# Kernel optimization log

Hardware: AMD Instinct MI355X
Metric: run time of the kernel (lower is better)

The kernel has to match this reference:

```python
import jax, jax.numpy as jnp
import numpy as np

N_NODES = 100000
N_EDGES = 1600000
HIDDEN = 128


def setup_inputs() -> dict:
    key = jax.random.key(0)
    k_x, k_w1, k_w2, k_v, k_i, k_o = jax.random.split(key, 6)
    x = jax.random.normal(k_x, (N_NODES, HIDDEN), dtype=jnp.float32)
    # gate1/gate2 are Linear(hidden,1,bias=False); store their weight rows as vectors
    w1 = jax.random.normal(k_w1, (HIDDEN,), dtype=jnp.float32) * 0.1
    w2 = jax.random.normal(k_w2, (HIDDEN,), dtype=jnp.float32) * 0.1
    adj_vals = jax.random.uniform(k_v, (N_EDGES,), dtype=jnp.float32)
    in_idx = jax.random.randint(k_i, (N_EDGES,), 0, N_NODES, dtype=jnp.int32)
    out_idx = jax.random.randint(k_o, (N_EDGES,), 0, N_NODES, dtype=jnp.int32)
    return {"x": x, "w1": w1, "w2": w2, "adj_vals": adj_vals,
            "in_idx": in_idx, "out_idx": out_idx}


def reference(x, w1, w2, adj_vals, in_idx, out_idx):
    # per-node gate scalars: x1 = gate1(x), x2 = gate2(x)  -> [N]
    x1 = x @ w1
    x2 = x @ w2
    # edge gate: tanh(x1[src] + x2[dst]) * adj_value  (dropout is identity in eval mode)
    m = jnp.tanh(x1[in_idx] + x2[out_idx]) * adj_vals  # [E]
    # sparse.mm(adj_alpha, x): out[i] = sum_{e: row(e)=i} m_e * x[col(e)]
    messages = m[:, None] * x[out_idx]                 # [E, d]
    result = jax.ops.segment_sum(messages, in_idx, num_segments=N_NODES)
    return result
```

## Files before the change

### kernel.cpp

```cpp
#include <hip/hip_runtime.h>

#define N_NODES 100000
#define N_EDGES 1600000
#define HIDDEN  128

#define NPB_SHIFT 9
#define NPB       512
#define NB        ((N_NODES + NPB - 1) / NPB)
#define PART_T    512
#define PART_EPT  16
#define PART_EPB  (PART_T * PART_EPT)
#define PART_B    ((N_EDGES + PART_EPB - 1) / PART_EPB)
#define HIST_EPT  16
#define HIST_EPB  (256 * HIST_EPT)
#define HIST_B    ((N_EDGES + HIST_EPB - 1) / HIST_EPB)
#define GATES_B   ((N_NODES * 32 + 255) / 256)
#define FINE_PE   20

#define SCAN_C 16
#define SCAN_T ((N_NODES + SCAN_C - 1) / SCAN_C)
#define SCAN_THREADS 6400
#define SCAN_B (SCAN_THREADS / 256)

__device__ __forceinline__ ushort f2bf(float f) {
    unsigned int u = __float_as_uint(f);
    u = (u + 0x7FFFu + ((u >> 16) & 1u)) >> 16;
    return (ushort)u;
}

__global__ void fagcn_zero(int* __restrict__ bcnt) {
    const int t = (int)threadIdx.x;
    if (t < NB) bcnt[t] = 0;
}

__global__ void fagcn_gates_hist(const float* __restrict__ x,
                                 const float* __restrict__ w1,
                                 const float* __restrict__ w2,
                                 const int*   __restrict__ in_idx,
                                 float* __restrict__ g1,
                                 float* __restrict__ g2,
                                 int*   __restrict__ bcnt,
                                 ushort* __restrict__ xh,
                                 int write_xh,
                                 int with_hist) {
    __shared__ int cnt[NB];
    if ((int)blockIdx.x < GATES_B) {
        const int tid  = blockIdx.x * 256 + (int)threadIdx.x;
        const int node = tid >> 5;
        const int hl   = (int)(threadIdx.x & 31);
        if (node >= N_NODES) return;

        const float4 xv  = *reinterpret_cast<const float4*>(x  + (size_t)node * HIDDEN + hl * 4);
        const float4 w1v = *reinterpret_cast<const float4*>(w1 + hl * 4);
        const float4 w2v = *reinterpret_cast<const float4*>(w2 + hl * 4);

        if (write_xh) {
            ushort4 h;
            h.x = f2bf(xv.x); h.y = f2bf(xv.y); h.z = f2bf(xv.z); h.w = f2bf(xv.w);
            *reinterpret_cast<ushort4*>(xh + (size_t)node * HIDDEN + hl * 4) = h;
        }

        float s1 = xv.x * w1v.x + xv.y * w1v.y + xv.z * w1v.z + xv.w * w1v.w;
        float s2 = xv.x * w2v.x + xv.y * w2v.y + xv.z * w2v.z + xv.w * w2v.w;

        #pragma unroll
        for (int off = 16; off > 0; off >>= 1) {
            s1 += __shfl_down(s1, off, 32);
            s2 += __shfl_down(s2, off, 32);
        }
        if (hl == 0) { g1[node] = s1; g2[node] = s2; }
    } else if (with_hist) {
        const int tid  = (int)threadIdx.x;
        const int base = ((int)blockIdx.x - GATES_B) * HIST_EPB + tid * HIST_EPT;
        for (int j = tid; j < NB; j += 256) cnt[j] = 0;
        __syncthreads();
        if (base < N_EDGES) {
            #pragma unroll
            for (int i = 0; i < 4; ++i) {
                const int4 v = *reinterpret_cast<const int4*>(in_idx + base + i * 4);
                atomicAdd(&cnt[v.x >> NPB_SHIFT], 1);
                atomicAdd(&cnt[v.y >> NPB_SHIFT], 1);
                atomicAdd(&cnt[v.z >> NPB_SHIFT], 1);
                atomicAdd(&cnt[v.w >> NPB_SHIFT], 1);
            }
        }
        __syncthreads();
        for (int j = tid; j < NB; j += 256)
            if (cnt[j]) atomicAdd(&bcnt[j], cnt[j]);
    }
}

__global__ void fagcn_scanb(const int* __restrict__ bcnt,
                            int* __restrict__ sbase,
                            int* __restrict__ bcur) {
    __shared__ int l[256];
    const int t = (int)threadIdx.x;
    const int c = (t < NB) ? bcnt[t] : 0;
    l[t] = c;
    __syncthreads();
    for (int off = 1; off < 256; off <<= 1) {
        int v = (t >= off) ? l[t - off] : 0;
        __syncthreads();
        l[t] += v;
        __syncthreads();
    }
    if (t < NB) { sbase[t] = l[t] - c; bcur[t] = 0; }
    if (t == NB - 1) sbase[NB] = l[t];
}

__global__ void fagcn_part(const float* __restrict__ adj,
                           const int*   __restrict__ in_idx,
                           const int*   __restrict__ out_idx,
                           const float* __restrict__ g1,
                           const float* __restrict__ g2,
                           const int*   __restrict__ sbase,
                           int*         __restrict__ bcur,
                           int2*        __restrict__ stage) {
    __shared__ int cnt[NB], lbase[NB], lcur[NB];
    const int tid  = (int)threadIdx.x;
    const int base = blockIdx.x * PART_EPB + tid * PART_EPT;

    for (int j = tid; j < NB; j += PART_T) { cnt[j] = 0; lcur[j] = 0; }
    __syncthreads();

    int s[PART_EPT];
    const bool act = (base < N_EDGES);
    if (act) {
        #pragma unroll
        for (int i = 0; i < PART_EPT / 4; ++i) {
            const int4 v = *reinterpret_cast<const int4*>(in_idx + base + i * 4);
            s[4 * i + 0] = v.x; s[4 * i + 1] = v.y;
            s[4 * i + 2] = v.z; s[4 * i + 3] = v.w;
        }
        #pragma unroll
        for (int i = 0; i < PART_EPT; ++i)
            atomicAdd(&cnt[s[i] >> NPB_SHIFT], 1);
    }
    __syncthreads();
    for (int j = tid; j < NB; j += PART_T)
        if (cnt[j] > 0) lbase[j] = sbase[j] + atomicAdd(&bcur[j], cnt[j]);
    __syncthreads();
    if (act) {
        #pragma unroll
        for (int i = 0; i < PART_EPT / 4; ++i) {
            const int4   d4 = *reinterpret_cast<const int4*>(out_idx + base + i * 4);
            const float4 a4 = *reinterpret_cast<const float4*>(adj + base + i * 4);
            const int   dd[4] = {d4.x, d4.y, d4.z, d4.w};
            const float aa[4] = {a4.x, a4.y, a4.z, a4.w};
            #pragma unroll
            for (int k = 0; k < 4; ++k) {
                const int src = s[4 * i + k];
                const int dst = dd[k];
                const float m = tanhf(g1[src] + g2[dst]) * aa[k];
                const int b   = src >> NPB_SHIFT;
                const int pos = lbase[b] + atomicAdd(&lcur[b], 1);
                stage[pos] = make_int2(((src & (NPB - 1)) << 17) | dst,
                                       __float_as_int(m));
            }
        }
    }
}

__global__ void fagcn_fine(const int2* __restrict__ stage,
                           const int*  __restrict__ sbase,
                           int*        __restrict__ offsets,
                           int2*       __restrict__ sedge) {
    __shared__ int cnt[NPB];
    __shared__ int cur[NPB];
    const int b = (int)blockIdx.x;
    const int t = (int)threadIdx.x;

    const int ebeg = sbase[b];
    const int eend = sbase[b + 1];

    cnt[t] = 0;
    __syncthreads();

    int2 pay[FINE_PE];
    #pragma unroll
    for (int i = 0; i < FINE_PE; ++i) {
        const int e = ebeg + t + i * NPB;
        if (e < eend) {
            pay[i] = stage[e];
            atomicAdd(&cnt[pay[i].x >> 17], 1);
        }
    }
    __syncthreads();

    const int c = cnt[t];
    for (int off = 1; off < NPB; off <<= 1) {
        int v = (t >= off) ? cnt[t - off] : 0;
        __syncthreads();
        cnt[t] += v;
        __syncthreads();
    }
    const int excl = cnt[t] - c;
    cur[t] = ebeg + excl;
    const int node = (b << NPB_SHIFT) + t;
    if (node < N_NODES) offsets[node] = ebeg + excl;
    if (b == (int)gridDim.x - 1 && t == 0) offsets[N_NODES] = N_EDGES;
    __syncthreads();

    #pragma unroll
    for (int i = 0; i < FINE_PE; ++i) {
        const int e = ebeg + t + i * NPB;
        if (e < eend) {
            const int pos = atomicAdd(&cur[pay[i].x >> 17], 1);
            sedge[pos] = make_int2(pay[i].x & 0x1FFFF, pay[i].y);
        }
    }
}

__device__ __forceinline__ void acc8(float* a, uint4 v, float m) {
    const unsigned int u[4] = {v.x, v.y, v.z, v.w};
    #pragma unroll
    for (int i = 0; i < 4; ++i) {
        const float lo = __uint_as_float(u[i] << 16);
        const float hi = __uint_as_float(u[i] & 0xFFFF0000u);
        a[2 * i]     += m * lo;
        a[2 * i + 1] += m * hi;
    }
}

__global__ void fagcn_gather_bf16(const ushort* __restrict__ xh,
                                  const int*   __restrict__ offsets,
                                  const int2*  __restrict__ sedge,
                                  float*       __restrict__ out,
                                  int node_beg, int node_end) {
    const int wave = node_beg + (int)((blockIdx.x * blockDim.x + threadIdx.x) >> 6);
    const int lane = (int)(threadIdx.x & 63);
    if (wave >= node_end) return;

    const int beg = offsets[wave];
    const int end = offsets[wave + 1];
    const int q   = lane >> 4;
    const int ql  = lane & 15;

    float a[8] = {0.f, 0.f, 0.f, 0.f, 0.f, 0.f, 0.f, 0.f};
    float b[8] = {0.f, 0.f, 0.f, 0.f, 0.f, 0.f, 0.f, 0.f};

    int e = beg + q;
    for (; e + 12 < end; e += 16) {
        const int2 ed0 = sedge[e];
        const int2 ed1 = sedge[e + 4];
        const int2 ed2 = sedge[e + 8];
        const int2 ed3 = sedge[e + 12];
        const uint4 v0 = *reinterpret_cast<const uint4*>(xh + (size_t)ed0.x * HIDDEN + ql * 8);
        const uint4 v1 = *reinterpret_cast<const uint4*>(xh + (size_t)ed1.x * HIDDEN + ql * 8);
        const uint4 v2 = *reinterpret_cast<const uint4*>(xh + (size_t)ed2.x * HIDDEN + ql * 8);
        const uint4 v3 = *reinterpret_cast<const uint4*>(xh + (size_t)ed3.x * HIDDEN + ql * 8);
        acc8(a, v0, __int_as_float(ed0.y));
        acc8(b, v1, __int_as_float(ed1.y));
        acc8(a, v2, __int_as_float(ed2.y));
        acc8(b, v3, __int_as_float(ed3.y));
    }
    for (; e < end; e += 4) {
        const int2 ed = sedge[e];
        const uint4 v = *reinterpret_cast<const uint4*>(xh + (size_t)ed.x * HIDDEN + ql * 8);
        acc8(a, v, __int_as_float(ed.y));
    }

    float r[8];
    #pragma unroll
    for (int i = 0; i < 8; ++i) r[i] = a[i] + b[i];
    #pragma unroll
    for (int i = 0; i < 8; ++i) r[i] += __shfl(r[i], lane ^ 16, 64);
    #pragma unroll
    for (int i = 0; i < 8; ++i) r[i] += __shfl(r[i], lane ^ 32, 64);

    if (lane < 16) {
        float* o = out + (size_t)wave * HIDDEN + ql * 8;
        float4 lo = {r[0], r[1], r[2], r[3]};
        float4 hi = {r[4], r[5], r[6], r[7]};
        *reinterpret_cast<float4*>(o)     = lo;
        *reinterpret_cast<float4*>(o + 4) = hi;
    }
}

__global__ void fagcn_hist(const int* __restrict__ in_idx,
                           int* __restrict__ counts) {
    const int e = blockIdx.x * blockDim.x + threadIdx.x;
    if (e < N_EDGES) atomicAdd(&counts[in_idx[e]], 1);
}

__global__ void fagcn_zero_nodes(int* __restrict__ counts) {
    const int i = blockIdx.x * blockDim.x + threadIdx.x;
    if (i < N_NODES) counts[i] = 0;
}

__global__ void fagcn_scan1(const int* __restrict__ counts,
                            int* __restrict__ tsum) {
    const int t = blockIdx.x * blockDim.x + threadIdx.x;
    if (t >= SCAN_THREADS) return;
    int s = 0;
    if (t < SCAN_T) {
        const int beg = t * SCAN_C;
        const int end = (beg + SCAN_C < N_NODES) ? beg + SCAN_C : N_NODES;
        for (int i = beg; i < end; ++i) s += counts[i];
    }
    tsum[t] = s;
}

__global__ void fagcn_scan2(int* __restrict__ tsum) {
    __shared__ int lsum[1024];
    const int t = (int)threadIdx.x;
    const int C = (SCAN_THREADS + 1023) / 1024;
    const int beg = t * C;
    const int end = (beg + C < SCAN_THREADS) ? beg + C : SCAN_THREADS;
    int s = 0;
    for (int i = beg; i < end; ++i) s += tsum[i];
    lsum[t] = s;
    __syncthreads();
    for (int off = 1; off < 1024; off <<= 1) {
        int v = (t >= off) ? lsum[t - off] : 0;
        __syncthreads();
        lsum[t] += v;
        __syncthreads();
    }
    int prefix = (t == 0) ? 0 : lsum[t - 1];
    for (int i = beg; i < end; ++i) {
        const int v = tsum[i];
        tsum[i] = prefix;
        prefix += v;
    }
}

__global__ void fagcn_scan3(int* counts,
                            const int* __restrict__ tsum,
                            int* __restrict__ offsets) {
    const int t = blockIdx.x * blockDim.x + threadIdx.x;
    if (t >= SCAN_T) return;
    const int beg = t * SCAN_C;
    const int end = (beg + SCAN_C < N_NODES) ? beg + SCAN_C : N_NODES;
    int prefix = tsum[t];
    for (int i = beg; i < end; ++i) {
        const int c = counts[i];
        offsets[i] = prefix;
        prefix += c;
        counts[i] = 0;
    }
    if (t == 0) offsets[N_NODES] = N_EDGES;
}

__global__ void fagcn_bin(const float* __restrict__ adj,
                          const int*   __restrict__ in_idx,
                          const int*   __restrict__ out_idx,
                          const float* __restrict__ g1,
                          const float* __restrict__ g2,
                          const int*   __restrict__ offsets,
                          int*         __restrict__ cursor,
                          int2*        __restrict__ sedge) {
    const int e = blockIdx.x * blockDim.x + threadIdx.x;
    if (e >= N_EDGES) return;
    const int src = in_idx[e];
    const int dst = out_idx[e];
    const float m = tanhf(g1[src] + g2[dst]) * adj[e];
    const int pos = offsets[src] + atomicAdd(&cursor[src], 1);
    sedge[pos] = make_int2(dst, __float_as_int(m));
}

__global__ void fagcn_gather_f32(const float* __restrict__ x,
                                 const int*   __restrict__ offsets,
                                 const int2*  __restrict__ sedge,
                                 float*       __restrict__ out) {
    const int wave = (int)((blockIdx.x * blockDim.x + threadIdx.x) >> 6);
    const int lane = (int)(threadIdx.x & 63);
    if (wave >= N_NODES) return;
    const int beg  = offsets[wave];
    const int end  = offsets[wave + 1];
    const int half = lane >> 5;
    const int hl   = lane & 31;
    float4 a0 = {0.f, 0.f, 0.f, 0.f};
    float4 a1 = {0.f, 0.f, 0.f, 0.f};
    int e = beg + half;
    for (; e + 2 < end; e += 4) {
        const int2 ed0 = sedge[e];
        const int2 ed1 = sedge[e + 2];
        const float m0 = __int_as_float(ed0.y);
        const float m1 = __int_as_float(ed1.y);
        const float4 v0 = *reinterpret_cast<const float4*>(x + (size_t)ed0.x * HIDDEN + hl * 4);
        const float4 v1 = *reinterpret_cast<const float4*>(x + (size_t)ed1.x * HIDDEN + hl * 4);
        a0.x += m0 * v0.x; a0.y += m0 * v0.y; a0.z += m0 * v0.z; a0.w += m0 * v0.w;
        a1.x += m1 * v1.x; a1.y += m1 * v1.y; a1.z += m1 * v1.z; a1.w += m1 * v1.w;
    }
    for (; e < end; e += 2) {
        const int2 ed = sedge[e];
        const float m = __int_as_float(ed.y);
        const float4 v = *reinterpret_cast<const float4*>(x + (size_t)ed.x * HIDDEN + hl * 4);
        a0.x += m * v.x; a0.y += m * v.y; a0.z += m * v.z; a0.w += m * v.w;
    }
    float4 a;
    a.x = a0.x + a1.x; a.y = a0.y + a1.y; a.z = a0.z + a1.z; a.w = a0.w + a1.w;
    a.x += __shfl(a.x, lane ^ 32, 64);
    a.y += __shfl(a.y, lane ^ 32, 64);
    a.z += __shfl(a.z, lane ^ 32, 64);
    a.w += __shfl(a.w, lane ^ 32, 64);
    if (half == 0) {
        *reinterpret_cast<float4*>(out + (size_t)wave * HIDDEN + hl * 4) = a;
    }
}

extern "C" void kernel_launch(void* const* d_in, const int* in_sizes, int n_in,
                              void* d_out, int out_size, void* d_ws, size_t ws_size,
                              hipStream_t stream) {
    const float* x        = (const float*)d_in[0];
    const float* w1       = (const float*)d_in[1];
    const float* w2       = (const float*)d_in[2];
    const float* adj_vals = (const float*)d_in[3];
    const int*   in_idx   = (const int*)d_in[4];
    const int*   out_idx  = (const int*)d_in[5];
    float* out = (float*)d_out;

    ushort* xh      = (ushort*)d_ws;
    int2*   sedge   = (int2*)(xh + (size_t)N_NODES * HIDDEN);
    int2*   stage   = sedge + N_EDGES;
    float*  g1      = (float*)(stage + N_EDGES);
    float*  g2      = g1 + N_NODES;
    int*    offsets = (int*)(g2 + N_NODES);
    int*    cursor  = offsets + N_NODES + 1;
    int*    tsum    = cursor + N_NODES;
    int*    bcnt    = tsum + SCAN_THREADS;
    int*    sbase   = bcnt + NB;
    int*    bcur    = sbase + NB + 1;

    const size_t need_full = (size_t)((char*)(bcur + NB) - (char*)d_ws);
    const size_t need_old  = need_full - (size_t)N_EDGES * 8;
    const int full_path = (ws_size >= need_full);
    const int bf16_ok   = (ws_size >= need_old);

    if (full_path) {
        fagcn_zero<<<1, 256, 0, stream>>>(bcnt);
        fagcn_gates_hist<<<GATES_B + HIST_B, 256, 0, stream>>>(
            x, w1, w2, in_idx, g1, g2, bcnt, xh, 1, 1);
        fagcn_scanb<<<1, 256, 0, stream>>>(bcnt, sbase, bcur);
        fagcn_part<<<PART_B, PART_T, 0, stream>>>(
            adj_vals, in_idx, out_idx, g1, g2, sbase, bcur, stage);
        fagcn_fine<<<NB, NPB, 0, stream>>>(stage, sbase, offsets, sedge);
        const int half_nodes = N_NODES / 2;
        fagcn_gather_bf16<<<(half_nodes + 3) / 4, 256, 0, stream>>>(
            xh, offsets, sedge, out, 0, half_nodes);
        fagcn_gather_bf16<<<(N_NODES - half_nodes + 3) / 4, 256, 0, stream>>>(
            xh, offsets, sedge, out, half_nodes, N_NODES);
    } else {
        if (!bf16_ok) sedge = (int2*)d_ws;
        fagcn_gates_hist<<<GATES_B, 256, 0, stream>>>(
            x, w1, w2, in_idx, g1, g2, bcnt, xh, bf16_ok, 0);
        fagcn_zero_nodes<<<(N_NODES + 255) / 256, 256, 0, stream>>>(cursor);
        fagcn_hist<<<(N_EDGES + 255) / 256, 256, 0, stream>>>(in_idx, cursor);
        fagcn_scan1<<<SCAN_B, 256, 0, stream>>>(cursor, tsum);
        fagcn_scan2<<<1, 1024, 0, stream>>>(tsum);
        fagcn_scan3<<<SCAN_B, 256, 0, stream>>>(cursor, tsum, offsets);
        fagcn_bin<<<(N_EDGES + 255) / 256, 256, 0, stream>>>(
            adj_vals, in_idx, out_idx, g1, g2, offsets, cursor, sedge);
        if (bf16_ok) {
            fagcn_gather_bf16<<<(N_NODES + 3) / 4, 256, 0, stream>>>(
                xh, offsets, sedge, out, 0, N_NODES);
        } else {
            fagcn_gather_f32<<<(N_NODES + 3) / 4, 256, 0, stream>>>(
                x, offsets, sedge, out);
        }
    }
}
```

Measured before the change: 159.3 us.

## Move edge gate tanh computation from partition into gather kernels

The per-edge gate tanh(g1[src]+g2[dst])*adj is no longer computed in the partition/bin kernels. The gather kernels now compute it, loading g1 once per destination row and g2 per edge, while the staged payload carries the raw adjacency value. This takes two random gathers and a tanh out of the scatter-heavy partition kernel, which is latency-bound on atomics. The cost is that the gather kernel recomputes the gate redundantly in each of its 16 lanes per edge group and adds an extra random g2 load per edge. The shift is also changed to unsigned so the top bit of the packed key is handled correctly.

```diff
diff --git a/kernel.cpp b/kernel.cpp
--- a/kernel.cpp
+++ b/kernel.cpp
@@ -111,8 +111,6 @@
 __global__ void fagcn_part(const float* __restrict__ adj,
                            const int*   __restrict__ in_idx,
                            const int*   __restrict__ out_idx,
-                           const float* __restrict__ g1,
-                           const float* __restrict__ g2,
                            const int*   __restrict__ sbase,
                            int*         __restrict__ bcur,
                            int2*        __restrict__ stage) {
@@ -150,12 +148,10 @@
             #pragma unroll
             for (int k = 0; k < 4; ++k) {
                 const int src = s[4 * i + k];
-                const int dst = dd[k];
-                const float m = tanhf(g1[src] + g2[dst]) * aa[k];
                 const int b   = src >> NPB_SHIFT;
                 const int pos = lbase[b] + atomicAdd(&lcur[b], 1);
-                stage[pos] = make_int2(((src & (NPB - 1)) << 17) | dst,
-                                       __float_as_int(m));
+                stage[pos] = make_int2(((src & (NPB - 1)) << 17) | dd[k],
+                                       __float_as_int(aa[k]));
             }
         }
     }
@@ -182,7 +178,7 @@
         const int e = ebeg + t + i * NPB;
         if (e < eend) {
             pay[i] = stage[e];
-            atomicAdd(&cnt[pay[i].x >> 17], 1);
+            atomicAdd(&cnt[(unsigned)pay[i].x >> 17], 1);
         }
     }
     __syncthreads();
@@ -205,7 +201,7 @@
     for (int i = 0; i < FINE_PE; ++i) {
         const int e = ebeg + t + i * NPB;
         if (e < eend) {
-            const int pos = atomicAdd(&cur[pay[i].x >> 17], 1);
+            const int pos = atomicAdd(&cur[(unsigned)pay[i].x >> 17], 1);
             sedge[pos] = make_int2(pay[i].x & 0x1FFFF, pay[i].y);
         }
     }
@@ -223,6 +219,8 @@
 }
 
 __global__ void fagcn_gather_bf16(const ushort* __restrict__ xh,
+                                  const float* __restrict__ g1,
+                                  const float* __restrict__ g2,
                                   const int*   __restrict__ offsets,
                                   const int2*  __restrict__ sedge,
                                   float*       __restrict__ out,
@@ -235,6 +233,7 @@
     const int end = offsets[wave + 1];
     const int q   = lane >> 4;
     const int ql  = lane & 15;
+    const float g1w = g1[wave];
 
     float a[8] = {0.f, 0.f, 0.f, 0.f, 0.f, 0.f, 0.f, 0.f};
     float b[8] = {0.f, 0.f, 0.f, 0.f, 0.f, 0.f, 0.f, 0.f};
@@ -245,19 +244,24 @@
         const int2 ed1 = sedge[e + 4];
         const int2 ed2 = sedge[e + 8];
         const int2 ed3 = sedge[e + 12];
+        const float G0 = g2[ed0.x];
+        const float G1 = g2[ed1.x];
+        const float G2 = g2[ed2.x];
+        const float G3 = g2[ed3.x];
         const uint4 v0 = *reinterpret_cast<const uint4*>(xh + (size_t)ed0.x * HIDDEN + ql * 8);
         const uint4 v1 = *reinterpret_cast<const uint4*>(xh + (size_t)ed1.x * HIDDEN + ql * 8);
         const uint4 v2 = *reinterpret_cast<const uint4*>(xh + (size_t)ed2.x * HIDDEN + ql * 8);
         const uint4 v3 = *reinterpret_cast<const uint4*>(xh + (size_t)ed3.x * HIDDEN + ql * 8);
-        acc8(a, v0, __int_as_float(ed0.y));
-        acc8(b, v1, __int_as_float(ed1.y));
-        acc8(a, v2, __int_as_float(ed2.y));
-        acc8(b, v3, __int_as_float(ed3.y));
+        acc8(a, v0, tanhf(g1w + G0) * __int_as_float(ed0.y));
+        acc8(b, v1, tanhf(g1w + G1) * __int_as_float(ed1.y));
+        acc8(a, v2, tanhf(g1w + G2) * __int_as_float(ed2.y));
+        acc8(b, v3, tanhf(g1w + G3) * __int_as_float(ed3.y));
     }
     for (; e < end; e += 4) {
         const int2 ed = sedge[e];
+        const float m = tanhf(g1w + g2[ed.x]) * __int_as_float(ed.y);
         const uint4 v = *reinterpret_cast<const uint4*>(xh + (size_t)ed.x * HIDDEN + ql * 8);
-        acc8(a, v, __int_as_float(ed.y));
+        acc8(a, v, m);
     }
 
     float r[8];
@@ -345,21 +349,19 @@
 __global__ void fagcn_bin(const float* __restrict__ adj,
                           const int*   __restrict__ in_idx,
                           const int*   __restrict__ out_idx,
-                          const float* __restrict__ g1,
-                          const float* __restrict__ g2,
                           const int*   __restrict__ offsets,
                           int*         __restrict__ cursor,
                           int2*        __restrict__ sedge) {
     const int e = blockIdx.x * blockDim.x + threadIdx.x;
     if (e >= N_EDGES) return;
     const int src = in_idx[e];
-    const int dst = out_idx[e];
-    const float m = tanhf(g1[src] + g2[dst]) * adj[e];
     const int pos = offsets[src] + atomicAdd(&cursor[src], 1);
-    sedge[pos] = make_int2(dst, __float_as_int(m));
+    sedge[pos] = make_int2(out_idx[e], __float_as_int(adj[e]));
 }
 
 __global__ void fagcn_gather_f32(const float* __restrict__ x,
+                                 const float* __restrict__ g1,
+                                 const float* __restrict__ g2,
                                  const int*   __restrict__ offsets,
                                  const int2*  __restrict__ sedge,
                                  float*       __restrict__ out) {
@@ -370,14 +372,15 @@
     const int end  = offsets[wave + 1];
     const int half = lane >> 5;
     const int hl   = lane & 31;
+    const float g1w = g1[wave];
     float4 a0 = {0.f, 0.f, 0.f, 0.f};
     float4 a1 = {0.f, 0.f, 0.f, 0.f};
     int e = beg + half;
     for (; e + 2 < end; e += 4) {
         const int2 ed0 = sedge[e];
         const int2 ed1 = sedge[e + 2];
-        const float m0 = __int_as_float(ed0.y);
-        const float m1 = __int_as_float(ed1.y);
+        const float m0 = tanhf(g1w + g2[ed0.x]) * __int_as_float(ed0.y);
+        const float m1 = tanhf(g1w + g2[ed1.x]) * __int_as_float(ed1.y);
         const float4 v0 = *reinterpret_cast<const float4*>(x + (size_t)ed0.x * HIDDEN + hl * 4);
         const float4 v1 = *reinterpret_cast<const float4*>(x + (size_t)ed1.x * HIDDEN + hl * 4);
         a0.x += m0 * v0.x; a0.y += m0 * v0.y; a0.z += m0 * v0.z; a0.w += m0 * v0.w;
@@ -385,7 +388,7 @@
     }
     for (; e < end; e += 2) {
         const int2 ed = sedge[e];
-        const float m = __int_as_float(ed.y);
+        const float m = tanhf(g1w + g2[ed.x]) * __int_as_float(ed.y);
         const float4 v = *reinterpret_cast<const float4*>(x + (size_t)ed.x * HIDDEN + hl * 4);
         a0.x += m * v.x; a0.y += m * v.y; a0.z += m * v.z; a0.w += m * v.w;
     }
@@ -434,13 +437,13 @@
             x, w1, w2, in_idx, g1, g2, bcnt, xh, 1, 1);
         fagcn_scanb<<<1, 256, 0, stream>>>(bcnt, sbase, bcur);
         fagcn_part<<<PART_B, PART_T, 0, stream>>>(
-            adj_vals, in_idx, out_idx, g1, g2, sbase, bcur, stage);
+            adj_vals, in_idx, out_idx, sbase, bcur, stage);
         fagcn_fine<<<NB, NPB, 0, stream>>>(stage, sbase, offsets, sedge);
         const int half_nodes = N_NODES / 2;
         fagcn_gather_bf16<<<(half_nodes + 3) / 4, 256, 0, stream>>>(
-            xh, offsets, sedge, out, 0, half_nodes);
+            xh, g1, g2, offsets, sedge, out, 0, half_nodes);
         fagcn_gather_bf16<<<(N_NODES - half_nodes + 3) / 4, 256, 0, stream>>>(
-            xh, offsets, sedge, out, half_nodes, N_NODES);
+            xh, g1, g2, offsets, sedge, out, half_nodes, N_NODES);
     } else {
         if (!bf16_ok) sedge = (int2*)d_ws;
         fagcn_gates_hist<<<GATES_B, 256, 0, stream>>>(
@@ -451,13 +454,13 @@
         fagcn_scan2<<<1, 1024, 0, stream>>>(tsum);
         fagcn_scan3<<<SCAN_B, 256, 0, stream>>>(cursor, tsum, offsets);
         fagcn_bin<<<(N_EDGES + 255) / 256, 256, 0, stream>>>(
-            adj_vals, in_idx, out_idx, g1, g2, offsets, cursor, sedge);
+            adj_vals, in_idx, out_idx, offsets, cursor, sedge);
         if (bf16_ok) {
             fagcn_gather_bf16<<<(N_NODES + 3) / 4, 256, 0, stream>>>(
-                xh, offsets, sedge, out, 0, N_NODES);
+                xh, g1, g2, offsets, sedge, out, 0, N_NODES);
         } else {
             fagcn_gather_f32<<<(N_NODES + 3) / 4, 256, 0, stream>>>(
-                x, offsets, sedge, out);
-        }
-    }
-}
+                x, g1, g2, offsets, sedge, out);
+        }
+    }
+}
```

Result: no change. 159.6 us (+0.2%).
